# Kernel optimization log

Measured on AMD Instinct MI355X. Metric: run time of the kernel, lower is better.

The kernel has to match this reference:

```python
import jax, jax.numpy as jnp
import numpy as np

N, E = 100000, 3200000
IN_DIM, PRED_DIM, REL_NUM = 128, 16, 50
H, L = 4, 3          # heads per layer, num_layers
NEG_SLOPE = 0.2      # SALayer attention leaky_relu slope


def setup_inputs() -> dict:
    key = jax.random.key(0)
    ks = jax.random.split(key, 9)
    hid = IN_DIM // 2
    return {
        "inputs": jax.random.normal(ks[0], (N, IN_DIM), jnp.float32),
        "centrality": jax.random.uniform(ks[1], (N,), jnp.float32),
        # per-head scoring MLP: Linear(in,in/2) -> ReLU -> Linear(in/2,1)
        "W1": jax.random.normal(ks[2], (H, hid, IN_DIM), jnp.float32) * 0.05,
        "b1": jnp.zeros((H, hid), jnp.float32),
        "W2": jax.random.normal(ks[3], (H, hid), jnp.float32) * 0.05,
        "b2": jnp.zeros((H,), jnp.float32),
        "rel_emb": jax.random.normal(ks[4], (REL_NUM, PRED_DIM), jnp.float32),
        # per-layer predicate->attention projection (pred_dim -> heads)
        "W_pred": jax.random.normal(ks[5], (L, PRED_DIM, H), jnp.float32) * 0.1,
        "gamma": jnp.ones((1, H), jnp.float32),
        "beta": jnp.zeros((1, H), jnp.float32),
        "edge_types": jax.random.randint(ks[6], (E,), 0, REL_NUM),
        "src": jax.random.randint(ks[7], (E,), 0, N),
        "dst": jax.random.randint(ks[8], (E,), 0, N),
    }


def _edge_softmax(e, dst, n):
    # numerically stable softmax over incoming edges of each dst node, per head
    m = jax.ops.segment_max(e, dst, num_segments=n)          # (N,H)
    ex = jnp.exp(e - m[dst])                                  # (E,H)
    s = jax.ops.segment_sum(ex, dst, num_segments=n)          # (N,H)
    return ex / s[dst]


def reference(inputs, centrality, W1, b1, W2, b2, rel_emb, W_pred,
              gamma, beta, edge_types, src, dst):
    n = inputs.shape[0]
    # multi-head scoring MLPs -> per-node per-head scalar scores (N,H)
    hid = jax.nn.relu(jnp.einsum('ni,khi->nkh', inputs, W1) + b1)  # (N,H,hid)
    h = jnp.einsum('nkh,kh->nk', hid, W2) + b2                     # (N,H)
    ef = rel_emb[edge_types]                                       # (E,P)
    for l in range(L):
        # SALayer: predicate-based attention, edge softmax, aggregate src scores
        e = jax.nn.leaky_relu(ef @ W_pred[l], NEG_SLOPE)           # (E,H)
        a = _edge_softmax(e, dst, n)                               # (E,H)
        h = jax.nn.relu(jax.ops.segment_sum(a * h[src], dst, num_segments=n))
        if l != L - 1:
            # flatten(1).mean(-1,keepdim).repeat(1,H)
            h = jnp.repeat(jnp.mean(h, axis=-1, keepdims=True), H, axis=-1)
    logits = h  # (N,H)
    # centrality scaling: leaky_relu(((c*gamma+beta)*logits).mean(-1,keepdim))
    scaled = (centrality[:, None] * gamma + beta) * logits
    return jax.nn.leaky_relu(jnp.mean(scaled, axis=-1, keepdims=True), 0.01)
```

## Files before the change

### kernel.cpp

```cpp
#include <hip/hip_runtime.h>
#include <cstdint>
#include <cstddef>

#define NHEAD 4
#define HID 64
#define NCOL 256
#define INDIM 128
#define PREDDIM 16
#define RELNUM 50
#define NLAYER 3
#define ECHUNK 8192
#define DSHIFT 9
#define DPB 512
#define MAXBUCK 256
#define MAXCHUNK 512
#define SPLIT_BLOCKS 32
#define MLP_GRID 512

typedef _Float16 half8 __attribute__((ext_vector_type(8)));
typedef float float4v __attribute__((ext_vector_type(4)));
typedef const __attribute__((address_space(1))) void gvoid_t;
typedef __attribute__((address_space(3))) void lvoid_t;

__global__ __launch_bounds__(256, 2) void mlp_mfma_kernel(
    const float* __restrict__ X, const _Float16* __restrict__ Wh,
    const _Float16* __restrict__ Wl, const float* __restrict__ b1,
    const float* __restrict__ W2, const float* __restrict__ b2,
    float* __restrict__ h0, int N)
{
    __shared__ float    Xf[64][128];
    __shared__ _Float16 hA[4][4][64][8];
    __shared__ _Float16 lA[4][4][64][8];

    const int tid  = threadIdx.x;
    const int w    = tid >> 6;
    const int lane = tid & 63;
    const int n16  = lane & 15;
    const int q    = lane >> 4;

    half8 bh[4][4], bl[4][4];
    float b1v[4], w2v[4];
    #pragma unroll
    for (int ct = 0; ct < 4; ct++) {
        const int c = w * 64 + ct * 16 + n16;
        const _Float16* pb = Wh + (size_t)c * INDIM + q * 8;
        const _Float16* pl = Wl + (size_t)c * INDIM + q * 8;
        #pragma unroll
        for (int ks = 0; ks < 4; ks++) {
            bh[ct][ks] = *reinterpret_cast<const half8*>(pb + ks * 32);
            bl[ct][ks] = *reinterpret_cast<const half8*>(pl + ks * 32);
        }
        b1v[ct] = b1[c];
        w2v[ct] = W2[c];
    }
    #pragma unroll
    for (int ct = 0; ct < 4; ct++) {
        #pragma unroll
        for (int ks = 0; ks < 4; ks++)
            asm volatile("" : "+v"(bh[ct][ks]), "+v"(bl[ct][ks]));
        asm volatile("" : "+v"(b1v[ct]), "+v"(w2v[ct]));
    }

    const float bk = b2[w];
    const int ntiles = (N + 63) >> 6;

    auto stage = [&](int tile) {
        #pragma unroll
        for (int i = 0; i < 8; i++) {
            const int lds_off = i * 4096 + w * 1024 + lane * 16;
            const int row  = lds_off >> 9;
            const int scol = (lds_off & 511) ^ ((row & 7) << 4);
            const int gn = min(tile * 64 + row, N - 1);
            const char* gsrc = (const char*)X + (size_t)gn * 512 + scol;
            char* ldst = (char*)(&Xf[0][0]) + lds_off;
            __builtin_amdgcn_global_load_lds((gvoid_t*)gsrc, (lvoid_t*)ldst,
                                             16, 0, 0);
        }
    };

    const int mg  = tid >> 2, sks = tid & 3;
    const int smt = mg >> 4,  sm  = mg & 15;
    const char* frow = (const char*)(&Xf[mg][0]);
    const int rswz = (mg & 7) << 4;

    auto convert = [&]() {
        #pragma unroll
        for (int qq = 0; qq < 4; qq++) {
            const int cb = sks * 128 + qq * 32;
            float4v r0 = *reinterpret_cast<const float4v*>(frow + (cb ^ rswz));
            float4v r1 = *reinterpret_cast<const float4v*>(frow + ((cb + 16) ^ rswz));
            half8 hv, lv;
            #pragma unroll
            for (int j = 0; j < 4; j++) {
                float x = r0[j];
                _Float16 hh = (_Float16)x;
                hv[j] = hh;
                lv[j] = (_Float16)((x - (float)hh) * 2048.0f);
                x = r1[j];
                hh = (_Float16)x;
                hv[4 + j] = hh;
                lv[4 + j] = (_Float16)((x - (float)hh) * 2048.0f);
            }
            const int slot = (qq * 16 + sm) ^ (2 * sks);
            *reinterpret_cast<half8*>(&hA[smt][sks][slot][0]) = hv;
            *reinterpret_cast<half8*>(&lA[smt][sks][slot][0]) = lv;
        }
    };

    int tile = blockIdx.x;
    if (tile >= ntiles) return;

    stage(tile);
    asm volatile("s_waitcnt vmcnt(0)" ::: "memory");
    __syncthreads();
    convert();
    __syncthreads();

    while (true) {
        const int nxt = tile + MLP_GRID;
        if (nxt < ntiles) stage(nxt);

        #pragma unroll 1
        for (int mt = 0; mt < 4; mt++) {
            half8 ah[4], al[4];
            #pragma unroll
            for (int kk = 0; kk < 4; kk++) {
                const int slot = lane ^ (2 * kk);
                ah[kk] = *reinterpret_cast<const half8*>(&hA[mt][kk][slot][0]);
                al[kk] = *reinterpret_cast<const half8*>(&lA[mt][kk][slot][0]);
            }

            float s[4] = {0.f, 0.f, 0.f, 0.f};
            #pragma unroll
            for (int ct = 0; ct < 4; ct++) {
                float4v acc = (float4v){0.f,0.f,0.f,0.f};
                float4v aca = (float4v){0.f,0.f,0.f,0.f};
                float4v acb = (float4v){0.f,0.f,0.f,0.f};
                #pragma unroll
                for (int kk = 0; kk < 4; kk++) {
                    acc = __builtin_amdgcn_mfma_f32_16x16x32_f16(ah[kk], bh[ct][kk], acc, 0, 0, 0);
                    aca = __builtin_amdgcn_mfma_f32_16x16x32_f16(ah[kk], bl[ct][kk], aca, 0, 0, 0);
                    acb = __builtin_amdgcn_mfma_f32_16x16x32_f16(al[kk], bh[ct][kk], acb, 0, 0, 0);
                }
                #pragma unroll
                for (int r = 0; r < 4; r++) {
                    float v = acc[r] + (aca[r] + acb[r]) * (1.0f / 2048.0f) + b1v[ct];
                    s[r] += fmaxf(v, 0.f) * w2v[ct];
                }
            }

            #pragma unroll
            for (int r = 0; r < 4; r++) {
                float v = s[r];
                v += __shfl_down(v, 8, 16);
                v += __shfl_down(v, 4, 16);
                v += __shfl_down(v, 2, 16);
                v += __shfl_down(v, 1, 16);
                if (n16 == 0) {
                    int node = tile * 64 + mt * 16 + q * 4 + r;
                    if (node < N) h0[(size_t)node * NHEAD + w] = v + bk;
                }
            }
        }

        if (nxt >= ntiles) break;

        asm volatile("s_waitcnt vmcnt(0)" ::: "memory");
        __syncthreads();
        convert();
        __syncthreads();
        tile = nxt;
    }
}

__global__ __launch_bounds__(1024) void bucket_count_fused_kernel(
    const int* __restrict__ dst, int* __restrict__ blockhist, int E,
    int nbuck, int nb,
    const float* __restrict__ rel_emb, const float* __restrict__ W_pred,
    float* __restrict__ wtab,
    const float* __restrict__ W1, _Float16* __restrict__ Wh,
    _Float16* __restrict__ Wl)
{
    __shared__ int hist[MAXBUCK];
    const int tid = threadIdx.x;
    const int bx  = blockIdx.x;

    if (bx < nb) {
        if (tid < MAXBUCK) hist[tid] = 0;
        __syncthreads();
        const int base = bx * ECHUNK;
        const int end  = min(base + ECHUNK, E);
        const int nvec = (end - base) >> 2;
        const int4* d4p = reinterpret_cast<const int4*>(dst + base);
        for (int g = tid; g < nvec; g += 1024) {
            int4 d = d4p[g];
            atomicAdd(&hist[d.x >> DSHIFT], 1);
            atomicAdd(&hist[d.y >> DSHIFT], 1);
            atomicAdd(&hist[d.z >> DSHIFT], 1);
            atomicAdd(&hist[d.w >> DSHIFT], 1);
        }
        for (int i = base + (nvec << 2) + tid; i < end; i += 1024)
            atomicAdd(&hist[dst[i] >> DSHIFT], 1);
        __syncthreads();
        if (tid < nbuck) blockhist[(size_t)tid * nb + bx] = hist[tid];
    } else if (bx == nb) {
        const int idx = tid;
        if (idx < NLAYER * RELNUM * NHEAD) {
            int h = idx & 3;
            int qq = idx >> 2;
            int t = qq % RELNUM;
            int l = qq / RELNUM;
            float acc = 0.f;
            #pragma unroll
            for (int p = 0; p < PREDDIM; p++)
                acc = fmaf(rel_emb[t * PREDDIM + p],
                           W_pred[l * PREDDIM * NHEAD + p * NHEAD + h], acc);
            float e = (acc >= 0.f) ? acc : 0.2f * acc;
            wtab[idx] = __expf(e);
        }
    } else {
        const int i = (bx - nb - 1) * 1024 + tid;
        float v = W1[i];
        _Float16 h = (_Float16)v;
        Wh[i] = h;
        Wl[i] = (_Float16)((v - (float)h) * 2048.0f);
    }
}

__global__ __launch_bounds__(512) void scan_chunks_kernel(
    const int* __restrict__ blockhist, int* __restrict__ blockbase,
    int* __restrict__ bucket_size, int nb)
{
    __shared__ int s[MAXCHUNK];
    const int b = blockIdx.x;
    const int t = threadIdx.x;
    int v = (t < nb) ? blockhist[(size_t)b * nb + t] : 0;
    s[t] = v;
    __syncthreads();
    for (int off = 1; off < MAXCHUNK; off <<= 1) {
        int u = (t >= off) ? s[t - off] : 0;
        __syncthreads();
        s[t] += u;
        __syncthreads();
    }
    if (t < nb) blockbase[(size_t)b * nb + t] = s[t] - v;
    if (t == MAXCHUNK - 1) bucket_size[b] = s[t];
}

__global__ __launch_bounds__(256) void scan_buckets_kernel(
    const int* __restrict__ bucket_size, int* __restrict__ bucket_start, int nbuck)
{
    __shared__ int s[256];
    const int t = threadIdx.x;
    int v = (t < nbuck) ? bucket_size[t] : 0;
    s[t] = v;
    __syncthreads();
    for (int off = 1; off < 256; off <<= 1) {
        int u = (t >= off) ? s[t - off] : 0;
        __syncthreads();
        s[t] += u;
        __syncthreads();
    }
    if (t < nbuck) bucket_start[t] = s[t] - v;
}

__global__ __launch_bounds__(1024) void bucket_scatter_kernel(
    const int* __restrict__ src, const int* __restrict__ dst,
    const int* __restrict__ types, const int* __restrict__ blockbase,
    const int* __restrict__ bucket_start, int* __restrict__ bucketed,
    int E, int nbuck, int nb)
{
    __shared__ int lbase[MAXBUCK];
    __shared__ int cur[MAXBUCK];
    const int tid = threadIdx.x;
    if (tid < MAXBUCK) {
        lbase[tid] = (tid < nbuck)
            ? blockbase[(size_t)tid * nb + blockIdx.x] + bucket_start[tid] : 0;
        cur[tid] = 0;
    }
    __syncthreads();
    const int base = blockIdx.x * ECHUNK;
    const int end  = min(base + ECHUNK, E);
    const int nvec = (end - base) >> 2;
    const int4* s4p = reinterpret_cast<const int4*>(src + base);
    const int4* d4p = reinterpret_cast<const int4*>(dst + base);
    const int4* t4p = reinterpret_cast<const int4*>(types + base);
    for (int g = tid; g < nvec; g += 1024) {
        int4 sv = s4p[g], dv = d4p[g], tv = t4p[g];
        int b, r;
        b = dv.x >> DSHIFT; r = atomicAdd(&cur[b], 1);
        bucketed[lbase[b] + r] = sv.x | (tv.x << 17) | ((dv.x & (DPB - 1)) << 23);
        b = dv.y >> DSHIFT; r = atomicAdd(&cur[b], 1);
        bucketed[lbase[b] + r] = sv.y | (tv.y << 17) | ((dv.y & (DPB - 1)) << 23);
        b = dv.z >> DSHIFT; r = atomicAdd(&cur[b], 1);
        bucketed[lbase[b] + r] = sv.z | (tv.z << 17) | ((dv.z & (DPB - 1)) << 23);
        b = dv.w >> DSHIFT; r = atomicAdd(&cur[b], 1);
        bucketed[lbase[b] + r] = sv.w | (tv.w << 17) | ((dv.w & (DPB - 1)) << 23);
    }
    for (int i = base + (nvec << 2) + tid; i < end; i += 1024) {
        int d = dst[i];
        int b = d >> DSHIFT;
        int r = atomicAdd(&cur[b], 1);
        bucketed[lbase[b] + r] = src[i] | (types[i] << 17) | ((d & (DPB - 1)) << 23);
    }
}

__global__ __launch_bounds__(1024) void bucket_to_csr_kernel(
    const int* __restrict__ bucket_start, const int* __restrict__ bucket_size,
    const int* __restrict__ bucketed, int* __restrict__ sorted,
    int* __restrict__ row_start, int* __restrict__ deg, int N)
{
    __shared__ int cnt[DPB];
    __shared__ int sc[DPB];
    __shared__ int rs[DPB];
    __shared__ int cur[DPB];
    const int tid = threadIdx.x;
    const int b   = blockIdx.x;
    const int d0  = b << DSHIFT;
    const int nd  = min(DPB, N - d0);
    const int s0  = bucket_start[b];
    const int ne  = bucket_size[b];

    if (tid < DPB) { cnt[tid] = 0; cur[tid] = 0; }
    __syncthreads();
    for (int i = tid; i < ne; i += 1024)
        atomicAdd(&cnt[((unsigned)bucketed[s0 + i] >> 23) & (DPB - 1)], 1);
    __syncthreads();
    int v = 0;
    if (tid < DPB) { v = cnt[tid]; sc[tid] = v; }
    __syncthreads();
    for (int off = 1; off < DPB; off <<= 1) {
        int u = (tid < DPB && tid >= off) ? sc[tid - off] : 0;
        __syncthreads();
        if (tid < DPB) sc[tid] += u;
        __syncthreads();
    }
    if (tid < DPB) {
        int ex = sc[tid] - v;
        rs[tid] = s0 + ex;
        if (tid < nd) {
            row_start[d0 + tid] = s0 + ex;
            deg[d0 + tid] = v;
        }
    }
    __syncthreads();
    for (int i = tid; i < ne; i += 1024) {
        int pk = bucketed[s0 + i];
        int d  = ((unsigned)pk >> 23) & (DPB - 1);
        int r  = atomicAdd(&cur[d], 1);
        sorted[rs[d] + r] = pk & 0x7FFFFF;
    }
}

template <int MODE>
__global__ __launch_bounds__(256) void agg_kernel(
    const int* __restrict__ row_start, const int* __restrict__ deg,
    const int* __restrict__ sorted, const float* __restrict__ wt_l,
    const float* __restrict__ hin, float* __restrict__ hout,
    const float* __restrict__ centrality, const float* __restrict__ gamma,
    const float* __restrict__ beta, int N)
{
    __shared__ float4 wt4[RELNUM];
    for (int i = threadIdx.x; i < RELNUM; i += blockDim.x)
        wt4[i] = reinterpret_cast<const float4*>(wt_l)[i];
    __syncthreads();

    int gid = blockIdx.x * blockDim.x + threadIdx.x;
    int d = gid >> 2, j = gid & 3;
    if (d >= N) return;

    int b = row_start[d], n = deg[d];
    float n0 = 0.f, n1 = 0.f, n2 = 0.f, n3 = 0.f;
    float d0 = 0.f, d1 = 0.f, d2 = 0.f, d3 = 0.f;
    for (int i = j; i < n; i += 4) {
        int pk = sorted[b + i];
        int s = pk & 0x1FFFF;
        int t = pk >> 17;
        float4 w4 = wt4[t];
        if (MODE == 0) {
            float4 h4 = *reinterpret_cast<const float4*>(hin + (size_t)s * NHEAD);
            n0 = fmaf(w4.x, h4.x, n0); n1 = fmaf(w4.y, h4.y, n1);
            n2 = fmaf(w4.z, h4.z, n2); n3 = fmaf(w4.w, h4.w, n3);
        } else {
            float hv = hin[s];
            n0 = fmaf(w4.x, hv, n0); n1 = fmaf(w4.y, hv, n1);
            n2 = fmaf(w4.z, hv, n2); n3 = fmaf(w4.w, hv, n3);
        }
        d0 += w4.x; d1 += w4.y; d2 += w4.z; d3 += w4.w;
    }

    #pragma unroll
    for (int k = 1; k <= 2; k <<= 1) {
        n0 += __shfl_xor(n0, k); n1 += __shfl_xor(n1, k);
        n2 += __shfl_xor(n2, k); n3 += __shfl_xor(n3, k);
        d0 += __shfl_xor(d0, k); d1 += __shfl_xor(d1, k);
        d2 += __shfl_xor(d2, k); d3 += __shfl_xor(d3, k);
    }

    if (j == 0) {
        float r0 = (n > 0) ? fmaxf(n0 / d0, 0.f) : 0.f;
        float r1 = (n > 0) ? fmaxf(n1 / d1, 0.f) : 0.f;
        float r2 = (n > 0) ? fmaxf(n2 / d2, 0.f) : 0.f;
        float r3 = (n > 0) ? fmaxf(n3 / d3, 0.f) : 0.f;
        if (MODE == 2) {
            float c = centrality[d];
            r0 *= (c * gamma[0] + beta[0]);
            r1 *= (c * gamma[1] + beta[1]);
            r2 *= (c * gamma[2] + beta[2]);
            r3 *= (c * gamma[3] + beta[3]);
        }
        float m = (r0 + r1 + r2 + r3) * 0.25f;
        if (MODE < 2) hout[d] = m;
        else          hout[d] = (m > 0.f) ? m : 0.01f * m;
    }
}

extern "C" void kernel_launch(void* const* d_in, const int* in_sizes, int n_in,
                              void* d_out, int out_size, void* d_ws, size_t ws_size,
                              hipStream_t stream)
{
    const float* X          = (const float*)d_in[0];
    const float* centrality = (const float*)d_in[1];
    const float* W1         = (const float*)d_in[2];
    const float* b1         = (const float*)d_in[3];
    const float* W2         = (const float*)d_in[4];
    const float* b2         = (const float*)d_in[5];
    const float* rel_emb    = (const float*)d_in[6];
    const float* W_pred     = (const float*)d_in[7];
    const float* gamma      = (const float*)d_in[8];
    const float* beta       = (const float*)d_in[9];
    const int*   edge_types = (const int*)d_in[10];
    const int*   src        = (const int*)d_in[11];
    const int*   dst        = (const int*)d_in[12];
    float* out = (float*)d_out;

    const int N = in_sizes[1];
    const int E = in_sizes[10];
    const int nbuck = (N + DPB - 1) / DPB;
    const int eb = (E + ECHUNK - 1) / ECHUNK;

    char* ws = (char*)d_ws;
    size_t off = 0;
    auto alloc = [&](size_t bytes) -> void* {
        void* p = ws + off;
        off = (off + bytes + 255) & ~(size_t)255;
        return p;
    };
    int*   deg       = (int*)alloc((size_t)N * 4);
    int*   row_start = (int*)alloc((size_t)N * 4);
    int*   bsize     = (int*)alloc((size_t)MAXBUCK * 4);
    int*   bstart    = (int*)alloc((size_t)MAXBUCK * 4);
    int*   blockhist = (int*)alloc((size_t)nbuck * eb * 4);
    int*   blockbase = (int*)alloc((size_t)nbuck * eb * 4);
    int*   bucketed  = (int*)alloc((size_t)E * 4);
    int*   sorted    = (int*)alloc((size_t)E * 4);
    float* wtab      = (float*)alloc((size_t)NLAYER * RELNUM * NHEAD * 4);
    float* h0        = (float*)alloc((size_t)N * NHEAD * 4);
    float* hs        = (float*)alloc((size_t)N * 4);
    float* hs2       = (float*)alloc((size_t)N * 4);
    _Float16* Wh     = (_Float16*)alloc((size_t)NCOL * INDIM * 2);
    _Float16* Wl     = (_Float16*)alloc((size_t)NCOL * INDIM * 2);
    (void)ws_size; (void)n_in; (void)out_size;

    bucket_count_fused_kernel<<<eb + 1 + SPLIT_BLOCKS, 1024, 0, stream>>>(
        dst, blockhist, E, nbuck, eb, rel_emb, W_pred, wtab, W1, Wh, Wl);
    scan_chunks_kernel<<<nbuck, MAXCHUNK, 0, stream>>>(blockhist, blockbase, bsize, eb);
    scan_buckets_kernel<<<1, 256, 0, stream>>>(bsize, bstart, nbuck);
    bucket_scatter_kernel<<<eb, 1024, 0, stream>>>(src, dst, edge_types, blockbase,
                                                   bstart, bucketed, E, nbuck, eb);
    bucket_to_csr_kernel<<<nbuck, 1024, 0, stream>>>(bstart, bsize, bucketed, sorted,
                                                     row_start, deg, N);

    mlp_mfma_kernel<<<MLP_GRID, 256, 0, stream>>>(X, Wh, Wl, b1, W2, b2, h0, N);

    const int ab = (N * NHEAD + 255) / 256;
    agg_kernel<0><<<ab, 256, 0, stream>>>(row_start, deg, sorted, wtab + 0 * RELNUM * NHEAD,
                                          h0, hs, nullptr, nullptr, nullptr, N);
    agg_kernel<1><<<ab, 256, 0, stream>>>(row_start, deg, sorted, wtab + 1 * RELNUM * NHEAD,
                                          hs, hs2, nullptr, nullptr, nullptr, N);
    agg_kernel<2><<<ab, 256, 0, stream>>>(row_start, deg, sorted, wtab + 2 * RELNUM * NHEAD,
                                          hs2, out, centrality, gamma, beta, N);
}
```

Measured before the change: 274.5 us.

## Fuse three aggregation layers into one persistent kernel with grid barriers

Replaces the three per-layer aggregation launches with a single persistent kernel of 1792 blocks. The blocks loop over 64-node chunks and synchronise between layers with a software grid barrier built on atomics. This removes two launches and their tail drains, but adds barrier spin cost, and correctness depends on all 1792 blocks being co-resident (256 threads at 8 blocks per CU across 256 CUs). The barrier counter is reset inside an earlier kernel.

```diff
diff --git a/kernel.cpp b/kernel.cpp
--- a/kernel.cpp
+++ b/kernel.cpp
@@ -16,6 +16,7 @@
 #define MAXCHUNK 512
 #define SPLIT_BLOCKS 32
 #define MLP_GRID 512
+#define AGG_GRID 1792
 
 typedef _Float16 half8 __attribute__((ext_vector_type(8)));
 typedef float float4v __attribute__((ext_vector_type(4)));
@@ -179,7 +180,7 @@
     const float* __restrict__ rel_emb, const float* __restrict__ W_pred,
     float* __restrict__ wtab,
     const float* __restrict__ W1, _Float16* __restrict__ Wh,
-    _Float16* __restrict__ Wl)
+    _Float16* __restrict__ Wl, int* __restrict__ bar_cnt)
 {
     __shared__ int hist[MAXBUCK];
     const int tid = threadIdx.x;
@@ -204,6 +205,7 @@
         __syncthreads();
         if (tid < nbuck) blockhist[(size_t)tid * nb + bx] = hist[tid];
     } else if (bx == nb) {
+        if (tid == 1022) *bar_cnt = 0;
         const int idx = tid;
         if (idx < NLAYER * RELNUM * NHEAD) {
             int h = idx & 3;
@@ -352,66 +354,112 @@
     }
 }
 
-template <int MODE>
-__global__ __launch_bounds__(256) void agg_kernel(
+__device__ __forceinline__ void grid_barrier(int* cnt, int* gen, int nb)
+{
+    __shared__ int sg;
+    __syncthreads();
+    if (threadIdx.x == 0)
+        sg = __hip_atomic_load(gen, __ATOMIC_RELAXED, __HIP_MEMORY_SCOPE_AGENT);
+    __syncthreads();
+    const int g0 = sg;
+    if (threadIdx.x == 0) {
+        __threadfence();
+        if (atomicAdd(cnt, 1) == nb - 1) {
+            __hip_atomic_store(cnt, 0, __ATOMIC_RELAXED, __HIP_MEMORY_SCOPE_AGENT);
+            __hip_atomic_fetch_add(gen, 1, __ATOMIC_RELEASE, __HIP_MEMORY_SCOPE_AGENT);
+        } else {
+            while (__hip_atomic_load(gen, __ATOMIC_ACQUIRE, __HIP_MEMORY_SCOPE_AGENT) == g0)
+                __builtin_amdgcn_s_sleep(16);
+        }
+        __threadfence();
+    }
+    __syncthreads();
+}
+
+__global__ __launch_bounds__(256, 8) void agg_fused_kernel(
     const int* __restrict__ row_start, const int* __restrict__ deg,
-    const int* __restrict__ sorted, const float* __restrict__ wt_l,
-    const float* __restrict__ hin, float* __restrict__ hout,
+    const int* __restrict__ sorted, const float* __restrict__ wtab,
+    const float* __restrict__ h0, float* __restrict__ hs,
+    float* __restrict__ hs2, float* __restrict__ out,
     const float* __restrict__ centrality, const float* __restrict__ gamma,
-    const float* __restrict__ beta, int N)
+    const float* __restrict__ beta, int* __restrict__ bar_cnt,
+    int* __restrict__ bar_gen, int N)
 {
     __shared__ float4 wt4[RELNUM];
-    for (int i = threadIdx.x; i < RELNUM; i += blockDim.x)
-        wt4[i] = reinterpret_cast<const float4*>(wt_l)[i];
-    __syncthreads();
-
-    int gid = blockIdx.x * blockDim.x + threadIdx.x;
-    int d = gid >> 2, j = gid & 3;
-    if (d >= N) return;
-
-    int b = row_start[d], n = deg[d];
-    float n0 = 0.f, n1 = 0.f, n2 = 0.f, n3 = 0.f;
-    float d0 = 0.f, d1 = 0.f, d2 = 0.f, d3 = 0.f;
-    for (int i = j; i < n; i += 4) {
-        int pk = sorted[b + i];
-        int s = pk & 0x1FFFF;
-        int t = pk >> 17;
-        float4 w4 = wt4[t];
-        if (MODE == 0) {
-            float4 h4 = *reinterpret_cast<const float4*>(hin + (size_t)s * NHEAD);
-            n0 = fmaf(w4.x, h4.x, n0); n1 = fmaf(w4.y, h4.y, n1);
-            n2 = fmaf(w4.z, h4.z, n2); n3 = fmaf(w4.w, h4.w, n3);
-        } else {
-            float hv = hin[s];
-            n0 = fmaf(w4.x, hv, n0); n1 = fmaf(w4.y, hv, n1);
-            n2 = fmaf(w4.z, hv, n2); n3 = fmaf(w4.w, hv, n3);
-        }
-        d0 += w4.x; d1 += w4.y; d2 += w4.z; d3 += w4.w;
-    }
-
-    #pragma unroll
-    for (int k = 1; k <= 2; k <<= 1) {
-        n0 += __shfl_xor(n0, k); n1 += __shfl_xor(n1, k);
-        n2 += __shfl_xor(n2, k); n3 += __shfl_xor(n3, k);
-        d0 += __shfl_xor(d0, k); d1 += __shfl_xor(d1, k);
-        d2 += __shfl_xor(d2, k); d3 += __shfl_xor(d3, k);
-    }
-
-    if (j == 0) {
-        float r0 = (n > 0) ? fmaxf(n0 / d0, 0.f) : 0.f;
-        float r1 = (n > 0) ? fmaxf(n1 / d1, 0.f) : 0.f;
-        float r2 = (n > 0) ? fmaxf(n2 / d2, 0.f) : 0.f;
-        float r3 = (n > 0) ? fmaxf(n3 / d3, 0.f) : 0.f;
-        if (MODE == 2) {
-            float c = centrality[d];
-            r0 *= (c * gamma[0] + beta[0]);
-            r1 *= (c * gamma[1] + beta[1]);
-            r2 *= (c * gamma[2] + beta[2]);
-            r3 *= (c * gamma[3] + beta[3]);
-        }
-        float m = (r0 + r1 + r2 + r3) * 0.25f;
-        if (MODE < 2) hout[d] = m;
-        else          hout[d] = (m > 0.f) ? m : 0.01f * m;
+    const int tid = threadIdx.x;
+    const int j   = tid & 3;
+    const int nchunk = (N + 63) >> 6;
+
+    const float g0v = gamma[0], g1v = gamma[1], g2v = gamma[2], g3v = gamma[3];
+    const float be0 = beta[0],  be1 = beta[1],  be2 = beta[2],  be3 = beta[3];
+
+    for (int l = 0; l < NLAYER; l++) {
+        for (int i = tid; i < RELNUM; i += 256)
+            wt4[i] = reinterpret_cast<const float4*>(wtab + l * RELNUM * NHEAD)[i];
+        __syncthreads();
+
+        const float* hin  = (l == 0) ? h0  : (l == 1) ? hs  : hs2;
+        float*       hout = (l == 0) ? hs  : (l == 1) ? hs2 : out;
+
+        for (int c = blockIdx.x; c < nchunk; c += AGG_GRID) {
+            const int d = c * 64 + (tid >> 2);
+            if (d < N) {
+                int b = row_start[d], n = deg[d];
+                float n0 = 0.f, n1 = 0.f, n2 = 0.f, n3 = 0.f;
+                float d0 = 0.f, d1 = 0.f, d2 = 0.f, d3 = 0.f;
+                if (l == 0) {
+                    for (int i = j; i < n; i += 4) {
+                        int pk = sorted[b + i];
+                        int s = pk & 0x1FFFF;
+                        int t = pk >> 17;
+                        float4 w4 = wt4[t];
+                        float4 h4 = *reinterpret_cast<const float4*>(hin + (size_t)s * NHEAD);
+                        n0 = fmaf(w4.x, h4.x, n0); n1 = fmaf(w4.y, h4.y, n1);
+                        n2 = fmaf(w4.z, h4.z, n2); n3 = fmaf(w4.w, h4.w, n3);
+                        d0 += w4.x; d1 += w4.y; d2 += w4.z; d3 += w4.w;
+                    }
+                } else {
+                    for (int i = j; i < n; i += 4) {
+                        int pk = sorted[b + i];
+                        int s = pk & 0x1FFFF;
+                        int t = pk >> 17;
+                        float4 w4 = wt4[t];
+                        float hv = hin[s];
+                        n0 = fmaf(w4.x, hv, n0); n1 = fmaf(w4.y, hv, n1);
+                        n2 = fmaf(w4.z, hv, n2); n3 = fmaf(w4.w, hv, n3);
+                        d0 += w4.x; d1 += w4.y; d2 += w4.z; d3 += w4.w;
+                    }
+                }
+
+                #pragma unroll
+                for (int k = 1; k <= 2; k <<= 1) {
+                    n0 += __shfl_xor(n0, k); n1 += __shfl_xor(n1, k);
+                    n2 += __shfl_xor(n2, k); n3 += __shfl_xor(n3, k);
+                    d0 += __shfl_xor(d0, k); d1 += __shfl_xor(d1, k);
+                    d2 += __shfl_xor(d2, k); d3 += __shfl_xor(d3, k);
+                }
+
+                if (j == 0) {
+                    float r0 = (n > 0) ? fmaxf(n0 / d0, 0.f) : 0.f;
+                    float r1 = (n > 0) ? fmaxf(n1 / d1, 0.f) : 0.f;
+                    float r2 = (n > 0) ? fmaxf(n2 / d2, 0.f) : 0.f;
+                    float r3 = (n > 0) ? fmaxf(n3 / d3, 0.f) : 0.f;
+                    if (l == 2) {
+                        float cv = centrality[d];
+                        r0 *= (cv * g0v + be0);
+                        r1 *= (cv * g1v + be1);
+                        r2 *= (cv * g2v + be2);
+                        r3 *= (cv * g3v + be3);
+                    }
+                    float m = (r0 + r1 + r2 + r3) * 0.25f;
+                    if (l < 2) hout[d] = m;
+                    else       hout[d] = (m > 0.f) ? m : 0.01f * m;
+                }
+            }
+        }
+
+        if (l < NLAYER - 1)
+            grid_barrier(bar_cnt, bar_gen, AGG_GRID);
     }
 }
 
@@ -460,10 +508,13 @@
     float* hs2       = (float*)alloc((size_t)N * 4);
     _Float16* Wh     = (_Float16*)alloc((size_t)NCOL * INDIM * 2);
     _Float16* Wl     = (_Float16*)alloc((size_t)NCOL * INDIM * 2);
+    int*   bar_cnt   = (int*)alloc(4);
+    int*   bar_gen   = (int*)alloc(4);
     (void)ws_size; (void)n_in; (void)out_size;
 
     bucket_count_fused_kernel<<<eb + 1 + SPLIT_BLOCKS, 1024, 0, stream>>>(
-        dst, blockhist, E, nbuck, eb, rel_emb, W_pred, wtab, W1, Wh, Wl);
+        dst, blockhist, E, nbuck, eb, rel_emb, W_pred, wtab, W1, Wh, Wl,
+        bar_cnt);
     scan_chunks_kernel<<<nbuck, MAXCHUNK, 0, stream>>>(blockhist, blockbase, bsize, eb);
     scan_buckets_kernel<<<1, 256, 0, stream>>>(bsize, bstart, nbuck);
     bucket_scatter_kernel<<<eb, 1024, 0, stream>>>(src, dst, edge_types, blockbase,
@@ -473,11 +524,7 @@
 
     mlp_mfma_kernel<<<MLP_GRID, 256, 0, stream>>>(X, Wh, Wl, b1, W2, b2, h0, N);
 
-    const int ab = (N * NHEAD + 255) / 256;
-    agg_kernel<0><<<ab, 256, 0, stream>>>(row_start, deg, sorted, wtab + 0 * RELNUM * NHEAD,
-                                          h0, hs, nullptr, nullptr, nullptr, N);
-    agg_kernel<1><<<ab, 256, 0, stream>>>(row_start, deg, sorted, wtab + 1 * RELNUM * NHEAD,
-                                          hs, hs2, nullptr, nullptr, nullptr, N);
-    agg_kernel<2><<<ab, 256, 0, stream>>>(row_start, deg, sorted, wtab + 2 * RELNUM * NHEAD,
-                                          hs2, out, centrality, gamma, beta, N);
-}
+    agg_fused_kernel<<<AGG_GRID, 256, 0, stream>>>(
+        row_start, deg, sorted, wtab, h0, hs, hs2, out,
+        centrality, gamma, beta, bar_cnt, bar_gen, N);
+}
```

After: 706.6 us. +157.4%, slower.
